# Optimization experiments

Measured on AMD Instinct MI355X. Metric: run time of the kernel, lower is better.

The kernel has to match this reference:

```python
import jax, jax.numpy as jnp
import numpy as np

N_DIM = 32
N_HEADS = 4
HEAD_SIZE = N_DIM // N_HEADS  # 8


def setup_inputs() -> dict:
    key = jax.random.key(0)
    ks = jax.random.split(key, 9)
    B, T = 16, 2048
    s = 1.0 / np.sqrt(N_DIM)
    inp = {
        "x": jax.random.normal(ks[0], (B, T, N_DIM), dtype=jnp.float32),
        "Wq": jax.random.uniform(ks[1], (N_DIM, N_DIM), jnp.float32, -s, s),
        "bq": jax.random.uniform(ks[2], (N_DIM,), jnp.float32, -s, s),
        "Wk": jax.random.uniform(ks[3], (N_DIM, N_DIM), jnp.float32, -s, s),
        "bk": jax.random.uniform(ks[4], (N_DIM,), jnp.float32, -s, s),
        "Wv": jax.random.uniform(ks[5], (N_DIM, N_DIM), jnp.float32, -s, s),
        "bv": jax.random.uniform(ks[6], (N_DIM,), jnp.float32, -s, s),
        "Wp": jax.random.uniform(ks[7], (N_DIM, N_DIM), jnp.float32, -s, s),
        "bp": jax.random.uniform(ks[8], (N_DIM,), jnp.float32, -s, s),
    }
    return inp


def reference(x, Wq, bq, Wk, bk, Wv, bv, Wp, bp):
    b, t, c = x.shape
    # nn.Linear: y = x @ W^T + b
    def heads(W, bias):
        y = jnp.einsum("btc,dc->btd", x, W) + bias
        return y.reshape(b, t, N_HEADS, HEAD_SIZE).transpose(0, 2, 1, 3)  # [b,h,t,d]

    q = heads(Wq, bq)
    k = heads(Wk, bk)
    v = heads(Wv, bv)

    scores = jnp.einsum("bhqd,bhkd->bhqk", q, k) / np.sqrt(HEAD_SIZE)  # [b,h,t,t]
    causal = jnp.tril(jnp.ones((t, t), dtype=bool))
    scores = jnp.where(causal[None, None], scores, -jnp.inf)
    weights = jax.nn.softmax(scores, axis=-1)
    # dropout layers are identity in eval mode
    z = jnp.einsum("bhqk,bhkd->bhqd", weights, v)
    z = z.transpose(0, 2, 1, 3).reshape(b, t, N_DIM)
    z = jnp.einsum("btc,dc->btd", z, Wp) + bp
    return z
```

## Files before the change

kernel.cpp:

```cpp
#include <hip/hip_runtime.h>
#include <math.h>

#define BB 16
#define TT 2048
#define CC 32
#define HH 4
#define DD 8

#define KBS 2056
#define VRS 264
#define VBS (9 * VRS)
#define ZP 33

typedef __fp16 h2  __attribute__((ext_vector_type(2)));
typedef __fp16 h8  __attribute__((ext_vector_type(8)));
typedef float  fx16 __attribute__((ext_vector_type(16)));
typedef int    i4v __attribute__((ext_vector_type(4)));
typedef int    i2v __attribute__((ext_vector_type(2)));

__device__ __forceinline__ h2 pkh(float a, float b) {
#if __has_builtin(__builtin_amdgcn_cvt_pkrtz)
    return __builtin_amdgcn_cvt_pkrtz(a, b);
#else
    h2 r; r.x = (__fp16)a; r.y = (__fp16)b; return r;
#endif
}

__device__ __forceinline__ float fexp2(float x) {
#if __has_builtin(__builtin_amdgcn_exp2f)
    return __builtin_amdgcn_exp2f(x);
#else
    return exp2f(x);
#endif
}

__device__ __forceinline__ int h2bits(h2 v) { return __builtin_bit_cast(int, v); }

__device__ __forceinline__ h8 pk8(float4 a, float4 b) {
    i4v f;
    f.x = h2bits(pkh(a.x, a.y)); f.y = h2bits(pkh(a.z, a.w));
    f.z = h2bits(pkh(b.x, b.y)); f.w = h2bits(pkh(b.z, b.w));
    return __builtin_bit_cast(h8, f);
}

__device__ __forceinline__ void makeP(const fx16& S, bool last, int thr, int hi, h8* P) {
    float pe[16];
    #pragma unroll
    for (int r = 0; r < 16; r++) {
        const int ko = (r & 3) + 8 * (r >> 2);
        float sv = S[r];
        if (last) sv = (ko <= thr) ? sv : -INFINITY;
        pe[r] = fexp2(sv);
    }
    int Hh[8];
    #pragma unroll
    for (int i = 0; i < 8; i++) Hh[i] = h2bits(pkh(pe[2*i], pe[2*i+1]));
#if __has_builtin(__builtin_amdgcn_permlane32_swap)
    #pragma unroll
    for (int s = 0; s < 2; s++) {
        const int b0 = 4 * s;
        auto ra = __builtin_amdgcn_permlane32_swap(Hh[b0+0], Hh[b0+2], false, false);
        auto rb = __builtin_amdgcn_permlane32_swap(Hh[b0+1], Hh[b0+3], false, false);
        i2v pa = __builtin_bit_cast(i2v, ra);
        i2v pb = __builtin_bit_cast(i2v, rb);
        i4v f;
        f.x = pa.x; f.y = pb.x; f.z = pa.y; f.w = pb.y;
        P[s] = __builtin_bit_cast(h8, f);
    }
#else
    #pragma unroll
    for (int s = 0; s < 2; s++) {
        const int b0 = 4 * s;
        int own0 = hi ? Hh[b0+2] : Hh[b0+0];
        int own1 = hi ? Hh[b0+3] : Hh[b0+1];
        int snd0 = hi ? Hh[b0+0] : Hh[b0+2];
        int snd1 = hi ? Hh[b0+1] : Hh[b0+3];
        int rcv0 = __shfl_xor(snd0, 32);
        int rcv1 = __shfl_xor(snd1, 32);
        i4v f;
        f.x = hi ? rcv0 : own0;
        f.y = hi ? rcv1 : own1;
        f.z = hi ? own0 : rcv0;
        f.w = hi ? own1 : rcv1;
        P[s] = __builtin_bit_cast(h8, f);
    }
#endif
}

__global__ __launch_bounds__(192, 3) void qkv_kernel(
    const float* __restrict__ x,
    const float* __restrict__ Wq, const float* __restrict__ bq,
    const float* __restrict__ Wk, const float* __restrict__ bk,
    const float* __restrict__ Wv, const float* __restrict__ bv,
    __fp16* __restrict__ Qo, __fp16* __restrict__ Ko, __fp16* __restrict__ Vo)
{
    const int tid  = threadIdx.x;
    const int m    = tid >> 6;
    const int lane = tid & 63;
    const int qc   = lane & 31;
    const int hi   = lane >> 5;

    const int row = blockIdx.x * 32 + qc;
    const int b   = row >> 11, t = row & 2047;

    const float* W    = (m == 0) ? Wq : (m == 1) ? Wk : Wv;
    const float* bias = (m == 0) ? bq : (m == 1) ? bk : bv;

    const float* xr = x + (size_t)row * CC + 8 * hi;
    h8 B0 = pk8(*(const float4*)(xr),      *(const float4*)(xr + 4));
    h8 B1 = pk8(*(const float4*)(xr + 16), *(const float4*)(xr + 20));

    const float* wr = W + (size_t)qc * CC + 8 * hi;
    h8 A0 = pk8(*(const float4*)(wr),      *(const float4*)(wr + 4));
    h8 A1 = pk8(*(const float4*)(wr + 16), *(const float4*)(wr + 20));

    fx16 zc;
    #pragma unroll
    for (int i = 0; i < 16; i++) zc[i] = 0.0f;
    fx16 D = __builtin_amdgcn_mfma_f32_32x32x16_f16(A0, B0, zc, 0, 0, 0);
    D = __builtin_amdgcn_mfma_f32_32x32x16_f16(A1, B1, D, 0, 0, 0);

    float o[16];
    {
        float4 bb0 = *(const float4*)(bias + 0  + 4 * hi);
        float4 bb1 = *(const float4*)(bias + 8  + 4 * hi);
        float4 bb2 = *(const float4*)(bias + 16 + 4 * hi);
        float4 bb3 = *(const float4*)(bias + 24 + 4 * hi);
        const float* bbp[1];
        o[0] = D[0] + bb0.x; o[1] = D[1] + bb0.y; o[2]  = D[2]  + bb0.z; o[3]  = D[3]  + bb0.w;
        o[4] = D[4] + bb1.x; o[5] = D[5] + bb1.y; o[6]  = D[6]  + bb1.z; o[7]  = D[7]  + bb1.w;
        o[8] = D[8] + bb2.x; o[9] = D[9] + bb2.y; o[10] = D[10] + bb2.z; o[11] = D[11] + bb2.w;
        o[12] = D[12] + bb3.x; o[13] = D[13] + bb3.y; o[14] = D[14] + bb3.z; o[15] = D[15] + bb3.w;
        (void)bbp;
    }
    if (m == 0) {
        const float qs = 0.3535533905932738f * 1.4426950408889634f;
        #pragma unroll
        for (int r = 0; r < 16; r++) o[r] *= qs;
    }

    if (m == 2) {
        #pragma unroll
        for (int r = 0; r < 16; r++) {
            const int h = r >> 2, d = (r & 3) + 4 * hi;
            Vo[(((size_t)(b * HH + h)) * 9 + d) * TT + t] = (__fp16)o[r];
        }
        const int hA = hi ? 2 : 0, hB = hi ? 3 : 1;
        Vo[(((size_t)(b * HH + hA)) * 9 + 8) * TT + t] = (__fp16)1.0f;
        Vo[(((size_t)(b * HH + hB)) * 9 + 8) * TT + t] = (__fp16)1.0f;
    } else {
        int I0[4], I1[4];
        #pragma unroll
        for (int g = 0; g < 4; g++) {
            I0[g] = h2bits(pkh(o[4*g + 0], o[4*g + 1]));
            I1[g] = h2bits(pkh(o[4*g + 2], o[4*g + 3]));
        }
        i4v fr0, fr1, fr2, fr3;
#if __has_builtin(__builtin_amdgcn_permlane32_swap)
    #define MAKE_FRAG(g, out) { \
        auto ra = __builtin_amdgcn_permlane32_swap(I0[g], I1[g], false, false); \
        auto rb = __builtin_amdgcn_permlane32_swap(I1[g], I0[g], false, false); \
        i2v p1 = __builtin_bit_cast(i2v, ra); \
        i2v p2 = __builtin_bit_cast(i2v, rb); \
        i4v f; \
        f.x = hi ? p2.x : p1.x;   \
        f.y = hi ? p1.x : p2.x;   \
        f.z = hi ? p2.y : p1.y;   \
        f.w = hi ? p1.y : p2.y;   \
        out = f; }
#else
    #define MAKE_FRAG(g, out) { \
        int s0 = __shfl_xor(I0[g], 32); \
        int s1 = __shfl_xor(I1[g], 32); \
        i4v f; \
        f.x = hi ? s0 : I0[g]; \
        f.y = hi ? s1 : I1[g]; \
        f.z = hi ? I0[g] : s0; \
        f.w = hi ? I1[g] : s1; \
        out = f; }
#endif
        MAKE_FRAG(0, fr0); MAKE_FRAG(1, fr1); MAKE_FRAG(2, fr2); MAKE_FRAG(3, fr3);
    #undef MAKE_FRAG
        i4v fA = hi ? fr2 : fr0;
        i4v fB = hi ? fr3 : fr1;
        const int gA = hi ? 2 : 0, gB = hi ? 3 : 1;
        __fp16* O = (m == 0) ? Qo : Ko;
        *(i4v*)(O + ((size_t)(b * HH + gA) * TT + t) * DD) = fA;
        *(i4v*)(O + ((size_t)(b * HH + gB) * TT + t) * DD) = fB;
    }
}

__global__ __launch_bounds__(256, 2) void attn_kernel(
    const __fp16* __restrict__ Qg, const __fp16* __restrict__ Kg,
    const __fp16* __restrict__ Vg,
    const float* __restrict__ Wp, const float* __restrict__ bp,
    float* __restrict__ out)
{
    __shared__ __align__(16) __fp16 KsS[4 * KBS];
    __shared__ __align__(16) __fp16 VtS[4 * VBS];
    __shared__ float zbuf[64 * ZP];

    const int tid  = threadIdx.x;
    const int b    = blockIdx.x & 15;
    const int ip   = blockIdx.x >> 4;
    const int h    = tid >> 6;
    const int lane = tid & 63;
    const int qc   = lane & 31;
    const int hi   = lane >> 5;

    const int bh  = b * HH + h;
    const int qb1 = 32 * ip;
    const int qb2 = 32 * (63 - ip);
    const int keys_needed = qb2 + 32;
    const int nst = (keys_needed + 255) >> 8;

    h8 qf1, qf2;
    {
        h8 qz;
        #pragma unroll
        for (int i = 0; i < 8; i++) qz[i] = (__fp16)0.0f;
        h8 qa = *(const h8*)(Qg + ((size_t)bh * TT + qb1 + qc) * DD);
        h8 qb = *(const h8*)(Qg + ((size_t)bh * TT + qb2 + qc) * DD);
        qf1 = hi ? qz : qa;
        qf2 = hi ? qz : qb;
    }

    fx16 O1, O2, zc;
    #pragma unroll
    for (int i = 0; i < 16; i++) { O1[i] = 0.0f; O2[i] = 0.0f; zc[i] = 0.0f; }

    const int vrow = (qc < 9) ? qc : 8;
    const int thr  = qc - 4 * hi;

    const __fp16* kgl = Kg + (size_t)bh * TT * DD;
    const __fp16* vgl = Vg + (size_t)bh * 9 * TT;
    __fp16* kld = KsS + h * KBS;
    __fp16* vld = VtS + h * VBS;
    const __fp16* kb = kld + qc * DD;
    const __fp16* vb = vld + vrow * VRS + 8 * hi;

    i4v kpre[4], vpre[5];
    {
        const i4v* ks = (const i4v*)kgl;
        #pragma unroll
        for (int r = 0; r < 4; r++) kpre[r] = ks[lane + 64 * r];
        #pragma unroll
        for (int r = 0; r < 5; r++) {
            int i = lane + 64 * r; if (i > 287) i = 287;
            vpre[r] = *(const i4v*)(vgl + (i >> 5) * TT + (i & 31) * 8);
        }
    }

    for (int sti = 0; sti < nst; sti++) {
        const int st = sti * 256;
        {
            i4v* kd = (i4v*)kld;
            #pragma unroll
            for (int r = 0; r < 4; r++) kd[lane + 64 * r] = kpre[r];
            #pragma unroll
            for (int r = 0; r < 5; r++) {
                const int i = lane + 64 * r;
                if (i < 288) *(i4v*)(vld + (i >> 5) * VRS + (i & 31) * 8) = vpre[r];
            }
        }
        if (sti + 1 < nst) {
            const int st2 = st + 256;
            const i4v* ks = (const i4v*)(kgl + (size_t)st2 * DD);
            #pragma unroll
            for (int r = 0; r < 4; r++) kpre[r] = ks[lane + 64 * r];
            #pragma unroll
            for (int r = 0; r < 5; r++) {
                int i = lane + 64 * r; if (i > 287) i = 287;
                vpre[r] = *(const i4v*)(vgl + (i >> 5) * TT + st2 + (i & 31) * 8);
            }
        }

        const int kend = min(st + 256, keys_needed);
        for (int kt = st; kt < kend; kt += 32) {
            const bool a1 = (kt <= qb1);
            h8 kf = *(const h8*)(kb + (kt - st) * DD);

            h8 P1[2], P2[2];
            if (a1) {
                fx16 S = __builtin_amdgcn_mfma_f32_32x32x16_f16(kf, qf1, zc, 0, 0, 0);
                makeP(S, kt == qb1, thr, hi, P1);
            }
            {
                fx16 S = __builtin_amdgcn_mfma_f32_32x32x16_f16(kf, qf2, zc, 0, 0, 0);
                makeP(S, kt == qb2, thr, hi, P2);
            }
            #pragma unroll
            for (int s = 0; s < 2; s++) {
                h8 vf = *(const h8*)(vb + (kt - st) + 16 * s);
                if (a1) O1 = __builtin_amdgcn_mfma_f32_32x32x16_f16(vf, P1[s], O1, 0, 0, 0);
                O2 = __builtin_amdgcn_mfma_f32_32x32x16_f16(vf, P2[s], O2, 0, 0, 0);
            }
        }
    }

    {
        const float i1 = 1.0f / O1[4], i2 = 1.0f / O2[4];
        float* z1 = &zbuf[qc * ZP + h * DD + 4 * hi];
        float* z2 = &zbuf[(32 + qc) * ZP + h * DD + 4 * hi];
        z1[0] = O1[0]*i1; z1[1] = O1[1]*i1; z1[2] = O1[2]*i1; z1[3] = O1[3]*i1;
        z2[0] = O2[0]*i2; z2[1] = O2[1]*i2; z2[2] = O2[2]*i2; z2[3] = O2[3]*i2;
    }
    __syncthreads();

    {
        const int seg = tid >> 6;
        const int r = tid & 63;
        float zr[CC];
        #pragma unroll
        for (int c = 0; c < CC; c++) zr[c] = zbuf[r * ZP + c];
        float o[DD];
        #pragma unroll
        for (int d = 0; d < DD; d++) {
            const int dd = seg * DD + d;
            float acc = bp[dd];
            #pragma unroll
            for (int c = 0; c < CC; c++) acc += zr[c] * Wp[dd * CC + c];
            o[d] = acc;
        }
        const int qglob = (r < 32) ? (ip * 32 + r) : ((63 - ip) * 32 + (r - 32));
        float* dst = out + ((size_t)b * TT + qglob) * CC + seg * DD;
        ((float4*)dst)[0] = make_float4(o[0], o[1], o[2], o[3]);
        ((float4*)dst)[1] = make_float4(o[4], o[5], o[6], o[7]);
    }
}

extern "C" void kernel_launch(void* const* d_in, const int* in_sizes, int n_in,
                              void* d_out, int out_size, void* d_ws, size_t ws_size,
                              hipStream_t stream) {
    const float* x  = (const float*)d_in[0];
    const float* Wq = (const float*)d_in[1];
    const float* bq = (const float*)d_in[2];
    const float* Wk = (const float*)d_in[3];
    const float* bk = (const float*)d_in[4];
    const float* Wv = (const float*)d_in[5];
    const float* bv = (const float*)d_in[6];
    const float* Wp = (const float*)d_in[7];
    const float* bp = (const float*)d_in[8];
    float* out = (float*)d_out;

    const size_t NE = (size_t)BB * HH * TT * DD;
    __fp16* Qh = (__fp16*)d_ws;
    __fp16* Kh = Qh + NE;
    __fp16* Vt = Kh + NE;

    qkv_kernel<<<dim3(BB * TT / 32), 192, 0, stream>>>(x, Wq, bq, Wk, bk, Wv, bv, Qh, Kh, Vt);
    attn_kernel<<<dim3(BB * 32), 256, 0, stream>>>(Qh, Kh, Vt, Wp, bp, out);
}
```

Baseline: 106.0 us.

## Split attention key range across two wave groups per head and merge partials

The attention block grows from 4 to 8 waves, and the two wave groups of each head process disjoint halves of the key range for the query tile pair. Unnormalized outputs and row sums are written to separate shared buffers and combined before normalization and the output projection. The projection is redistributed so each thread computes 4 outputs. This targets low occupancy and the long serial key loop at the cost of extra shared memory, a larger block and merge overhead.

```diff
diff --git a/kernel.cpp b/kernel.cpp
--- a/kernel.cpp
+++ b/kernel.cpp
@@ -7,9 +7,9 @@
 #define HH 4
 #define DD 8
 
-#define KBS 2056
-#define VRS 264
-#define VBS (9 * VRS)
+#define KBS2 1040
+#define VRS2 136
+#define VBS2 (9 * VRS2)
 #define ZP 33
 
 typedef __fp16 h2  __attribute__((ext_vector_type(2)));
@@ -126,12 +126,10 @@
         float4 bb1 = *(const float4*)(bias + 8  + 4 * hi);
         float4 bb2 = *(const float4*)(bias + 16 + 4 * hi);
         float4 bb3 = *(const float4*)(bias + 24 + 4 * hi);
-        const float* bbp[1];
         o[0] = D[0] + bb0.x; o[1] = D[1] + bb0.y; o[2]  = D[2]  + bb0.z; o[3]  = D[3]  + bb0.w;
         o[4] = D[4] + bb1.x; o[5] = D[5] + bb1.y; o[6]  = D[6]  + bb1.z; o[7]  = D[7]  + bb1.w;
         o[8] = D[8] + bb2.x; o[9] = D[9] + bb2.y; o[10] = D[10] + bb2.z; o[11] = D[11] + bb2.w;
         o[12] = D[12] + bb3.x; o[13] = D[13] + bb3.y; o[14] = D[14] + bb3.z; o[15] = D[15] + bb3.w;
-        (void)bbp;
     }
     if (m == 0) {
         const float qs = 0.3535533905932738f * 1.4426950408889634f;
@@ -163,10 +161,10 @@
         i2v p1 = __builtin_bit_cast(i2v, ra); \
         i2v p2 = __builtin_bit_cast(i2v, rb); \
         i4v f; \
-        f.x = hi ? p2.x : p1.x;   \
-        f.y = hi ? p1.x : p2.x;   \
-        f.z = hi ? p2.y : p1.y;   \
-        f.w = hi ? p1.y : p2.y;   \
+        f.x = hi ? p2.x : p1.x; \
+        f.y = hi ? p1.x : p2.x; \
+        f.z = hi ? p2.y : p1.y; \
+        f.w = hi ? p1.y : p2.y; \
         out = f; }
 #else
     #define MAKE_FRAG(g, out) { \
@@ -190,20 +188,25 @@
     }
 }
 
-__global__ __launch_bounds__(256, 2) void attn_kernel(
+__global__ __launch_bounds__(512, 4) void attn_kernel(
     const __fp16* __restrict__ Qg, const __fp16* __restrict__ Kg,
     const __fp16* __restrict__ Vg,
     const float* __restrict__ Wp, const float* __restrict__ bp,
     float* __restrict__ out)
 {
-    __shared__ __align__(16) __fp16 KsS[4 * KBS];
-    __shared__ __align__(16) __fp16 VtS[4 * VBS];
-    __shared__ float zbuf[64 * ZP];
+    __shared__ __align__(16) __fp16 KsS[8 * KBS2];
+    __shared__ __align__(16) __fp16 VtS[8 * VBS2];
+    __shared__ float zA[64 * ZP];
+    __shared__ float zB[64 * ZP];
+    __shared__ float lA[64 * 4];
+    __shared__ float lB[64 * 4];
 
     const int tid  = threadIdx.x;
     const int b    = blockIdx.x & 15;
     const int ip   = blockIdx.x >> 4;
-    const int h    = tid >> 6;
+    const int w    = tid >> 6;
+    const int h    = w & 3;
+    const int hsel = w >> 2;
     const int lane = tid & 63;
     const int qc   = lane & 31;
     const int hi   = lane >> 5;
@@ -211,8 +214,9 @@
     const int bh  = b * HH + h;
     const int qb1 = 32 * ip;
     const int qb2 = 32 * (63 - ip);
-    const int keys_needed = qb2 + 32;
-    const int nst = (keys_needed + 255) >> 8;
+    const int stile = (ip < 15) ? (31 - ip) : 16;
+    const int ks = hsel ? stile * 32 : 0;
+    const int ke = hsel ? (64 - ip) * 32 : stile * 32;
 
     h8 qf1, qf2;
     {
@@ -234,48 +238,56 @@
 
     const __fp16* kgl = Kg + (size_t)bh * TT * DD;
     const __fp16* vgl = Vg + (size_t)bh * 9 * TT;
-    __fp16* kld = KsS + h * KBS;
-    __fp16* vld = VtS + h * VBS;
+    __fp16* kld = KsS + w * KBS2;
+    __fp16* vld = VtS + w * VBS2;
     const __fp16* kb = kld + qc * DD;
-    const __fp16* vb = vld + vrow * VRS + 8 * hi;
-
-    i4v kpre[4], vpre[5];
-    {
-        const i4v* ks = (const i4v*)kgl;
-        #pragma unroll
-        for (int r = 0; r < 4; r++) kpre[r] = ks[lane + 64 * r];
-        #pragma unroll
-        for (int r = 0; r < 5; r++) {
-            int i = lane + 64 * r; if (i > 287) i = 287;
-            vpre[r] = *(const i4v*)(vgl + (i >> 5) * TT + (i & 31) * 8);
+    const __fp16* vb = vld + vrow * VRS2 + 8 * hi;
+
+    const int nst = (ke - ks + 127) >> 7;
+
+    i4v kpre[2], vpre[3];
+    {
+        #pragma unroll
+        for (int r = 0; r < 2; r++) {
+            int row = ks + lane + 64 * r; if (row > TT - 1) row = TT - 1;
+            kpre[r] = *(const i4v*)(kgl + (size_t)row * DD);
+        }
+        #pragma unroll
+        for (int r = 0; r < 3; r++) {
+            int i = lane + 64 * r; if (i > 143) i = 143;
+            int col = ks + (i & 15) * 8; if (col > TT - 8) col = TT - 8;
+            vpre[r] = *(const i4v*)(vgl + (i >> 4) * TT + col);
         }
     }
 
     for (int sti = 0; sti < nst; sti++) {
-        const int st = sti * 256;
+        const int st = ks + sti * 128;
         {
             i4v* kd = (i4v*)kld;
             #pragma unroll
-            for (int r = 0; r < 4; r++) kd[lane + 64 * r] = kpre[r];
-            #pragma unroll
-            for (int r = 0; r < 5; r++) {
+            for (int r = 0; r < 2; r++) kd[lane + 64 * r] = kpre[r];
+            #pragma unroll
+            for (int r = 0; r < 3; r++) {
                 const int i = lane + 64 * r;
-                if (i < 288) *(i4v*)(vld + (i >> 5) * VRS + (i & 31) * 8) = vpre[r];
+                if (i < 144) *(i4v*)(vld + (i >> 4) * VRS2 + (i & 15) * 8) = vpre[r];
             }
         }
         if (sti + 1 < nst) {
-            const int st2 = st + 256;
-            const i4v* ks = (const i4v*)(kgl + (size_t)st2 * DD);
-            #pragma unroll
-            for (int r = 0; r < 4; r++) kpre[r] = ks[lane + 64 * r];
-            #pragma unroll
-            for (int r = 0; r < 5; r++) {
-                int i = lane + 64 * r; if (i > 287) i = 287;
-                vpre[r] = *(const i4v*)(vgl + (i >> 5) * TT + st2 + (i & 31) * 8);
-            }
-        }
-
-        const int kend = min(st + 256, keys_needed);
+            const int st2 = st + 128;
+            #pragma unroll
+            for (int r = 0; r < 2; r++) {
+                int row = st2 + lane + 64 * r; if (row > TT - 1) row = TT - 1;
+                kpre[r] = *(const i4v*)(kgl + (size_t)row * DD);
+            }
+            #pragma unroll
+            for (int r = 0; r < 3; r++) {
+                int i = lane + 64 * r; if (i > 143) i = 143;
+                int col = st2 + (i & 15) * 8; if (col > TT - 8) col = TT - 8;
+                vpre[r] = *(const i4v*)(vgl + (i >> 4) * TT + col);
+            }
+        }
+
+        const int kend = min(st + 128, ke);
         for (int kt = st; kt < kend; kt += 32) {
             const bool a1 = (kt <= qb1);
             h8 kf = *(const h8*)(kb + (kt - st) * DD);
@@ -299,33 +311,40 @@
     }
 
     {
-        const float i1 = 1.0f / O1[4], i2 = 1.0f / O2[4];
-        float* z1 = &zbuf[qc * ZP + h * DD + 4 * hi];
-        float* z2 = &zbuf[(32 + qc) * ZP + h * DD + 4 * hi];
-        z1[0] = O1[0]*i1; z1[1] = O1[1]*i1; z1[2] = O1[2]*i1; z1[3] = O1[3]*i1;
-        z2[0] = O2[0]*i2; z2[1] = O2[1]*i2; z2[2] = O2[2]*i2; z2[3] = O2[3]*i2;
+        float* zW = hsel ? zB : zA;
+        float* lW = hsel ? lB : lA;
+        float* z1 = &zW[qc * ZP + h * DD + 4 * hi];
+        float* z2 = &zW[(32 + qc) * ZP + h * DD + 4 * hi];
+        z1[0] = O1[0]; z1[1] = O1[1]; z1[2] = O1[2]; z1[3] = O1[3];
+        z2[0] = O2[0]; z2[1] = O2[1]; z2[2] = O2[2]; z2[3] = O2[3];
+        lW[qc * 4 + h] = O1[4];
+        lW[(32 + qc) * 4 + h] = O2[4];
     }
     __syncthreads();
 
     {
         const int seg = tid >> 6;
         const int r = tid & 63;
+        float linv[4];
+        #pragma unroll
+        for (int hh = 0; hh < 4; hh++)
+            linv[hh] = 1.0f / (lA[r * 4 + hh] + lB[r * 4 + hh]);
         float zr[CC];
         #pragma unroll
-        for (int c = 0; c < CC; c++) zr[c] = zbuf[r * ZP + c];
-        float o[DD];
-        #pragma unroll
-        for (int d = 0; d < DD; d++) {
-            const int dd = seg * DD + d;
+        for (int c = 0; c < CC; c++)
+            zr[c] = (zA[r * ZP + c] + zB[r * ZP + c]) * linv[c >> 3];
+        float o[4];
+        #pragma unroll
+        for (int d = 0; d < 4; d++) {
+            const int dd = seg * 4 + d;
             float acc = bp[dd];
             #pragma unroll
             for (int c = 0; c < CC; c++) acc += zr[c] * Wp[dd * CC + c];
             o[d] = acc;
         }
         const int qglob = (r < 32) ? (ip * 32 + r) : ((63 - ip) * 32 + (r - 32));
-        float* dst = out + ((size_t)b * TT + qglob) * CC + seg * DD;
-        ((float4*)dst)[0] = make_float4(o[0], o[1], o[2], o[3]);
-        ((float4*)dst)[1] = make_float4(o[4], o[5], o[6], o[7]);
+        float* dst = out + ((size_t)b * TT + qglob) * CC + seg * 4;
+        *(float4*)dst = make_float4(o[0], o[1], o[2], o[3]);
     }
 }
 
@@ -349,5 +368,5 @@
     __fp16* Vt = Kh + NE;
 
     qkv_kernel<<<dim3(BB * TT / 32), 192, 0, stream>>>(x, Wq, bq, Wk, bk, Wv, bv, Qh, Kh, Vt);
-    attn_kernel<<<dim3(BB * 32), 256, 0, stream>>>(Qh, Kh, Vt, Wp, bp, out);
-}
+    attn_kernel<<<dim3(BB * 32), 512, 0, stream>>>(Qh, Kh, Vt, Wp, bp, out);
+}
```

New measurement: 105.4 us. Within noise of the previous version (-0.5%).
